# Optimization experiments

Hardware: AMD Instinct MI355X
Metric: run time of the kernel (lower is better)

Reference implementation:

```python
import jax, jax.numpy as jnp
import numpy as np

N_NODES = 50000
N_EDGES = 800000
N_GRAPHS = 256


def setup_inputs() -> dict:
    key = jax.random.key(0)
    ks = jax.random.split(key, 20)
    s = 0.05
    return {
        "x": jax.random.normal(ks[0], (N_NODES, 128), jnp.float32),
        "edge_index": jax.random.randint(ks[1], (2, N_EDGES), 0, N_NODES, jnp.int64),
        "batch_index": jnp.sort(jax.random.randint(ks[2], (N_NODES,), 0, N_GRAPHS, jnp.int64)),
        "mol_features": jax.random.normal(ks[3], (N_GRAPHS, 256), jnp.float32),
        "gcn_W": jax.random.normal(ks[4], (3, 128, 128), jnp.float32) * s,
        "gcn_b": jax.random.normal(ks[5], (3, 128), jnp.float32) * s,
        "gcn_out_W": jax.random.normal(ks[6], (128, 128), jnp.float32) * s,
        "gcn_out_b": jax.random.normal(ks[7], (128,), jnp.float32) * s,
        "mlp_W": jax.random.normal(ks[8], (2, 256, 256), jnp.float32) * s,
        "mlp_b": jax.random.normal(ks[9], (2, 256), jnp.float32) * s,
        "mlp_out_W": jax.random.normal(ks[10], (64, 256), jnp.float32) * s,
        "mlp_out_b": jax.random.normal(ks[11], (64,), jnp.float32) * s,
        "pred_W1": jax.random.normal(ks[12], (256, 192), jnp.float32) * s,
        "pred_b1": jax.random.normal(ks[13], (256,), jnp.float32) * s,
        "pred_W2": jax.random.normal(ks[14], (256, 256), jnp.float32) * s,
        "pred_b2": jax.random.normal(ks[15], (256,), jnp.float32) * s,
        "out_W": jax.random.normal(ks[16], (1, 256), jnp.float32) * s,
        "out_b": jax.random.normal(ks[17], (1,), jnp.float32) * s,
    }


def reference(x, edge_index, batch_index, mol_features,
              gcn_W, gcn_b, gcn_out_W, gcn_out_b,
              mlp_W, mlp_b, mlp_out_W, mlp_out_b,
              pred_W1, pred_b1, pred_W2, pred_b2, out_W, out_b):
    N = x.shape[0]
    E = edge_index.shape[1]
    G = mol_features.shape[0]
    row, col = edge_index[0], edge_index[1]

    # GCN normalization with self-loops (PyG gcn_norm, symmetric):
    # deg[i] = in-degree(i) + 1 (self loop); norm_e = d^-1/2[row] * d^-1/2[col]
    deg = jax.ops.segment_sum(jnp.ones((E,), x.dtype), col, num_segments=N) + 1.0
    dinv = jax.lax.rsqrt(deg)
    enorm = (dinv[row] * dinv[col])[:, None]     # [E,1]
    self_c = (dinv * dinv)[:, None]              # [N,1] self-loop coefficient

    h1 = x
    for i in range(gcn_W.shape[0]):
        h = h1 @ gcn_W[i].T                      # per-node transform [N,128]
        agg = jax.ops.segment_sum(h[row] * enorm, col, num_segments=N)
        h1 = jax.nn.relu(agg + self_c * h + gcn_b[i])
    h1 = h1 @ gcn_out_W.T + gcn_out_b            # final GCN-branch Linear (no relu)

    # global_mean_pool over batch_index -> [G,128]
    sums = jax.ops.segment_sum(h1, batch_index, num_segments=G)
    counts = jax.ops.segment_sum(jnp.ones((N,), x.dtype), batch_index, num_segments=G)
    h1 = sums / jnp.maximum(counts, 1.0)[:, None]

    # MLP branch: relu after every linear (including last)
    h2 = mol_features
    for i in range(mlp_W.shape[0]):
        h2 = jax.nn.relu(h2 @ mlp_W[i].T + mlp_b[i])
    h2 = jax.nn.relu(h2 @ mlp_out_W.T + mlp_out_b)

    h = jnp.concatenate([h1, h2], axis=1)        # [G,192]
    h = jax.nn.relu(h @ pred_W1.T + pred_b1)
    h = jax.nn.relu(h @ pred_W2.T + pred_b2)
    return h @ out_W.T + out_b                   # [G,1]
```

## Files before the change

kernel.cpp:

```cpp
#include <hip/hip_runtime.h>


typedef __attribute__((ext_vector_type(8))) short short8;
typedef __attribute__((ext_vector_type(4))) float f32x4;

#define BKT 64
#define SL 8
#define NBINBLK 256

__device__ __forceinline__ unsigned short f2bf(float f) {
    union { float f; unsigned u; } c; c.f = f;
    unsigned u = c.u;
    unsigned r = u + 0x7FFFu + ((u >> 16) & 1u);
    return (unsigned short)(r >> 16);
}
__device__ __forceinline__ float bflo(unsigned w) {
    union { unsigned u; float f; } c; c.u = w << 16; return c.f;
}
__device__ __forceinline__ float bfhi(unsigned w) {
    union { unsigned u; float f; } c; c.u = w & 0xFFFF0000u; return c.f;
}

__global__ void k_zero(int* ghist, float* pool, float* cnt, int* csr_pad,
                       int M, int N, int G) {
    int i = blockIdx.x * blockDim.x + threadIdx.x;
    if (i < M) ghist[i] = 0;
    if (i < G * 128) pool[i] = 0.f;
    if (i < G) cnt[i] = 0.f;
    if (i < 8) csr_pad[i] = 0;
}

__global__ __launch_bounds__(256) void k_hist(const int* __restrict__ col,
                                              int* __restrict__ ghist,
                                              int E, int C, int NBK) {
    __shared__ int h[784];
    int t = threadIdx.x;
    for (int i = t; i < NBK; i += 256) h[i] = 0;
    __syncthreads();
    const int x = blockIdx.x & (SL - 1);
    int e0 = blockIdx.x * C, e1 = min(E, e0 + C);
    for (int e = e0 + t; e < e1; e += 256) atomicAdd(&h[col[e] >> 6], 1);
    __syncthreads();
    for (int b = t; b < NBK; b += 256) {
        int c = h[b];
        if (c) atomicAdd(&ghist[b * SL + x], c);
    }
}

__global__ __launch_bounds__(256) void k_bscan(const int* __restrict__ ghist,
                                               int* __restrict__ gbase,
                                               int* __restrict__ cur,
                                               int* __restrict__ rowptr,
                                               int M, int N, int E) {
    __shared__ int ws[4];
    __shared__ int s_carry;
    int t = threadIdx.x, lane = t & 63, wv = t >> 6;
    if (t == 0) s_carry = 0;
    __syncthreads();
    for (int base = 0; base < M; base += 256) {
        int i = base + t;
        int v = (i < M) ? ghist[i] : 0;
        int x = v;
        #pragma unroll
        for (int off = 1; off < 64; off <<= 1) {
            int u = __shfl_up(x, off, 64);
            if (lane >= off) x += u;
        }
        if (lane == 63) ws[wv] = x;
        __syncthreads();
        int woff = 0;
        for (int w = 0; w < wv; ++w) woff += ws[w];
        int excl = s_carry + woff + (x - v);
        if (i < M) { gbase[i] = excl; cur[i] = excl; }
        __syncthreads();
        if (t == 255) s_carry = excl + v;
        __syncthreads();
    }
    if (t == 0) { gbase[M] = E; rowptr[N] = E; }
}

__global__ __launch_bounds__(256) void k_bin(const int* __restrict__ row,
                                             const int* __restrict__ col,
                                             int* __restrict__ cur,
                                             unsigned* __restrict__ gbin,
                                             int E, int C) {
    const int x = blockIdx.x & (SL - 1);
    int e0 = blockIdx.x * C, e1 = min(E, e0 + C);
    for (int e = e0 + threadIdx.x; e < e1; e += 256) {
        int c = col[e];
        int si = (c >> 6) * SL + x;
        int pos = atomicAdd(&cur[si], 1);
        gbin[pos] = (unsigned)row[e] | ((unsigned)(c & 63) << 16);
    }
}

__global__ __launch_bounds__(256) void k_csr(const unsigned* __restrict__ gbin,
                                             const int* __restrict__ gbase,
                                             int* __restrict__ rowptr,
                                             float* __restrict__ dinv,
                                             unsigned short* __restrict__ csrf,
                                             int N) {
    const int b = blockIdx.x, t = threadIdx.x;
    __shared__ int cnt[64], lcur[64];
    if (t < 64) cnt[t] = 0;
    __syncthreads();
    const int beg = gbase[b * SL], end = gbase[(b + 1) * SL];
    for (int i = beg + t; i < end; i += 256)
        atomicAdd(&cnt[gbin[i] >> 16], 1);
    __syncthreads();
    if (t < 64) {
        int v = cnt[t], x = v;
        #pragma unroll
        for (int off = 1; off < 64; off <<= 1) {
            int u = __shfl_up(x, off, 64);
            if (t >= off) x += u;
        }
        int excl = x - v;
        lcur[t] = excl;
        int node = b * 64 + t;
        if (node < N) {
            rowptr[node] = beg + excl;
            dinv[node] = rsqrtf((float)v + 1.0f);
        }
    }
    __syncthreads();
    for (int i = beg + t; i < end; i += 256) {
        unsigned v = gbin[i];
        int p = atomicAdd(&lcur[v >> 16], 1);
        csrf[beg + p] = (unsigned short)(v & 0xFFFFu);
    }
}

__global__ void k_castx(const float* __restrict__ x, const float* __restrict__ dinv,
                        unsigned short* __restrict__ xb, int total8) {
    int i = blockIdx.x * blockDim.x + threadIdx.x;
    if (i >= total8) return;
    float d = dinv[i >> 4];
    const float4* s = (const float4*)(x + (size_t)i * 8);
    float4 a = s[0], b = s[1];
    uint4 o;
    o.x = ((unsigned)f2bf(d * a.y) << 16) | f2bf(d * a.x);
    o.y = ((unsigned)f2bf(d * a.w) << 16) | f2bf(d * a.z);
    o.z = ((unsigned)f2bf(d * b.y) << 16) | f2bf(d * b.x);
    o.w = ((unsigned)f2bf(d * b.w) << 16) | f2bf(d * b.z);
    *(uint4*)(xb + (size_t)i * 8) = o;
}

__global__ void k_wcast(const float* __restrict__ gcnW, uint4* __restrict__ Wb) {
    int cid = blockIdx.x * 256 + threadIdx.x;
    if (cid >= 3 * 2048) return;
    int l = cid >> 11, rem = cid & 2047;
    int o = rem >> 4, c = rem & 15;
    const float4* s = (const float4*)(gcnW + (size_t)l * 16384 + o * 128 + c * 8);
    float4 a = s[0], b = s[1];
    uint4 v;
    v.x = ((unsigned)f2bf(a.y) << 16) | f2bf(a.x);
    v.y = ((unsigned)f2bf(a.w) << 16) | f2bf(a.z);
    v.z = ((unsigned)f2bf(b.y) << 16) | f2bf(b.x);
    v.w = ((unsigned)f2bf(b.w) << 16) | f2bf(b.z);
    Wb[(l << 11) | (o << 4) | (c ^ (o & 15))] = v;
}

__global__ __launch_bounds__(256) void k_agg(const unsigned short* __restrict__ h,
                                             unsigned short* __restrict__ y,
                                             const float* __restrict__ dinv,
                                             const int* __restrict__ rowptr,
                                             const unsigned short* __restrict__ csrf,
                                             int N) {
    const int lane = threadIdx.x & 63;
    const int n = blockIdx.x * 4 + (threadIdx.x >> 6);
    if (n >= N) return;
    const int fg = lane & 15;
    const int slot = lane >> 4;
    const int s = rowptr[n], e = rowptr[n + 1];

    float acc[8] = {0.f, 0.f, 0.f, 0.f, 0.f, 0.f, 0.f, 0.f};
    for (int base = s; base < e; base += 16) {
        int src_l = csrf[base + fg];
        #pragma unroll
        for (int i = 0; i < 4; ++i) {
            int j = i * 4 + slot;
            int src = __shfl(src_l, j, 16);
            uint4 v = *(const uint4*)(h + (size_t)src * 128 + fg * 8);
            bool ok = (base + j) < e;
            v.x = ok ? v.x : 0u; v.y = ok ? v.y : 0u;
            v.z = ok ? v.z : 0u; v.w = ok ? v.w : 0u;
            acc[0] += bflo(v.x); acc[1] += bfhi(v.x);
            acc[2] += bflo(v.y); acc[3] += bfhi(v.y);
            acc[4] += bflo(v.z); acc[5] += bfhi(v.z);
            acc[6] += bflo(v.w); acc[7] += bfhi(v.w);
        }
    }
    #pragma unroll
    for (int r = 0; r < 8; ++r) {
        acc[r] += __shfl_xor(acc[r], 16, 64);
        acc[r] += __shfl_xor(acc[r], 32, 64);
    }
    if (slot == 0) {
        float dn = dinv[n];
        uint4 hv = *(const uint4*)(h + (size_t)n * 128 + fg * 8);
        float sv[8] = {bflo(hv.x), bfhi(hv.x), bflo(hv.y), bfhi(hv.y),
                       bflo(hv.z), bfhi(hv.z), bflo(hv.w), bfhi(hv.w)};
        unsigned short ob[8];
        #pragma unroll
        for (int r = 0; r < 8; ++r) ob[r] = f2bf(dn * (acc[r] + sv[r]));
        uint4 o;
        o.x = ((unsigned)ob[1] << 16) | ob[0];
        o.y = ((unsigned)ob[3] << 16) | ob[2];
        o.z = ((unsigned)ob[5] << 16) | ob[4];
        o.w = ((unsigned)ob[7] << 16) | ob[6];
        *(uint4*)(y + (size_t)n * 128 + fg * 8) = o;
    }
}

__global__ __launch_bounds__(256) void k_mm(const unsigned short* __restrict__ A,
                                            const uint4* __restrict__ Wb,
                                            const float* __restrict__ bias,
                                            const float* __restrict__ dscale,
                                            unsigned short* __restrict__ C, int N) {
    __shared__ uint4 Wsh[2048];
    const int tid = threadIdx.x;
    #pragma unroll
    for (int it = 0; it < 8; ++it)
        Wsh[tid + it * 256] = Wb[tid + it * 256];

    const int lane = tid & 63;
    const int wv = tid >> 6;
    const int l15 = lane & 15, quad = lane >> 4;
    const int arow_i = blockIdx.x * 64 + wv * 16 + l15;
    const unsigned short* arow = A + (size_t)min(arow_i, N - 1) * 128;

    f32x4 acc[8];
    #pragma unroll
    for (int ct = 0; ct < 8; ++ct) acc[ct] = (f32x4){0.f, 0.f, 0.f, 0.f};

    __syncthreads();
    #pragma unroll
    for (int kiter = 0; kiter < 4; ++kiter) {
        short8 af = *(const short8*)(arow + kiter * 32 + quad * 8);
        const int cswz = (kiter * 4 + quad) ^ l15;
        #pragma unroll
        for (int ct = 0; ct < 8; ++ct) {
            short8 bf = *(const short8*)(&Wsh[((ct * 16 + l15) << 4) | cswz]);
            acc[ct] = __builtin_amdgcn_mfma_f32_16x16x32_bf16(af, bf, acc[ct], 0, 0, 0);
        }
    }

    const int rbase = blockIdx.x * 64 + wv * 16 + quad * 4;
    float ds[4];
    #pragma unroll
    for (int r = 0; r < 4; ++r) {
        int rr = rbase + r;
        ds[r] = (dscale && rr < N) ? dscale[rr] : 1.f;
    }
    #pragma unroll
    for (int ct = 0; ct < 8; ++ct) {
        int colc = ct * 16 + l15;
        float bcol = bias[colc];
        #pragma unroll
        for (int r = 0; r < 4; ++r) {
            int rr = rbase + r;
            if (rr < N) {
                float v = fmaxf(acc[ct][r] + bcol, 0.f) * ds[r];
                C[(size_t)rr * 128 + colc] = f2bf(v);
            }
        }
    }
}

__global__ __launch_bounds__(256) void k_pool(const unsigned short* __restrict__ h,
                                              const int* __restrict__ batch,
                                              float* __restrict__ pool,
                                              float* __restrict__ cnt, int N) {
    int t = threadIdx.x;
    int fg = t & 15, sg = t >> 4;
    int n0 = blockIdx.x * 512 + sg * 32;
    if (n0 >= N) return;
    int n1 = min(n0 + 32, N);
    int gprev = batch[n0];
    float racc[8] = {0.f, 0.f, 0.f, 0.f, 0.f, 0.f, 0.f, 0.f};
    float rcnt = 0.f;
    for (int n = n0; n < n1; ++n) {
        int g = batch[n];
        if (g != gprev) {
            float* dst = pool + (size_t)gprev * 128 + fg * 8;
            #pragma unroll
            for (int r = 0; r < 8; ++r) atomicAdd(dst + r, racc[r]);
            if (fg == 0) atomicAdd(&cnt[gprev], rcnt);
            #pragma unroll
            for (int r = 0; r < 8; ++r) racc[r] = 0.f;
            rcnt = 0.f; gprev = g;
        }
        uint4 v = *(const uint4*)(h + (size_t)n * 128 + fg * 8);
        racc[0] += bflo(v.x); racc[1] += bfhi(v.x);
        racc[2] += bflo(v.y); racc[3] += bfhi(v.y);
        racc[4] += bflo(v.z); racc[5] += bfhi(v.z);
        racc[6] += bflo(v.w); racc[7] += bfhi(v.w);
        rcnt += 1.f;
    }
    float* dst = pool + (size_t)gprev * 128 + fg * 8;
    #pragma unroll
    for (int r = 0; r < 8; ++r) atomicAdd(dst + r, racc[r]);
    if (fg == 0) atomicAdd(&cnt[gprev], rcnt);
}

__global__ __launch_bounds__(256) void k_head(
    const float* __restrict__ pool, const float* __restrict__ cnt,
    const float* __restrict__ gcnoW, const float* __restrict__ gcnob,
    const float* __restrict__ mol,
    const float* __restrict__ mlpW, const float* __restrict__ mlpb,
    const float* __restrict__ mloW, const float* __restrict__ mlob,
    const float* __restrict__ pW1, const float* __restrict__ pb1,
    const float* __restrict__ pW2, const float* __restrict__ pb2,
    const float* __restrict__ oW, const float* __restrict__ ob,
    float* __restrict__ out) {
    int g = blockIdx.x, t = threadIdx.x;
    __shared__ float s0[256], s1[256], s2[192], mean[128], red[256];

    s0[t] = mol[(size_t)g * 256 + t];
    if (t < 128) {
        float c = cnt[g];
        mean[t] = pool[(size_t)g * 128 + t] / fmaxf(c, 1.f);
    }
    __syncthreads();

    float acc = mlpb[t];
    {
        const float4* w = (const float4*)(mlpW + (size_t)t * 256);
        #pragma unroll 4
        for (int k4 = 0; k4 < 64; ++k4) {
            float4 wv = w[k4];
            acc += s0[k4*4+0]*wv.x + s0[k4*4+1]*wv.y + s0[k4*4+2]*wv.z + s0[k4*4+3]*wv.w;
        }
    }
    s1[t] = fmaxf(acc, 0.f);
    __syncthreads();

    acc = mlpb[256 + t];
    {
        const float4* w = (const float4*)(mlpW + 65536 + (size_t)t * 256);
        #pragma unroll 4
        for (int k4 = 0; k4 < 64; ++k4) {
            float4 wv = w[k4];
            acc += s1[k4*4+0]*wv.x + s1[k4*4+1]*wv.y + s1[k4*4+2]*wv.z + s1[k4*4+3]*wv.w;
        }
    }
    s0[t] = fmaxf(acc, 0.f);
    __syncthreads();

    if (t < 64) {
        float a2 = mlob[t];
        const float4* w = (const float4*)(mloW + (size_t)t * 256);
        #pragma unroll 4
        for (int k4 = 0; k4 < 64; ++k4) {
            float4 wv = w[k4];
            a2 += s0[k4*4+0]*wv.x + s0[k4*4+1]*wv.y + s0[k4*4+2]*wv.z + s0[k4*4+3]*wv.w;
        }
        s2[128 + t] = fmaxf(a2, 0.f);
    } else if (t < 192) {
        int o = t - 64;
        float a2 = gcnob[o];
        const float4* w = (const float4*)(gcnoW + (size_t)o * 128);
        #pragma unroll 4
        for (int k4 = 0; k4 < 32; ++k4) {
            float4 wv = w[k4];
            a2 += mean[k4*4+0]*wv.x + mean[k4*4+1]*wv.y + mean[k4*4+2]*wv.z + mean[k4*4+3]*wv.w;
        }
        s2[o] = a2;
    }
    __syncthreads();

    acc = pb1[t];
    {
        const float4* w = (const float4*)(pW1 + (size_t)t * 192);
        #pragma unroll 4
        for (int k4 = 0; k4 < 48; ++k4) {
            float4 wv = w[k4];
            acc += s2[k4*4+0]*wv.x + s2[k4*4+1]*wv.y + s2[k4*4+2]*wv.z + s2[k4*4+3]*wv.w;
        }
    }
    s1[t] = fmaxf(acc, 0.f);
    __syncthreads();

    acc = pb2[t];
    {
        const float4* w = (const float4*)(pW2 + (size_t)t * 256);
        #pragma unroll 4
        for (int k4 = 0; k4 < 64; ++k4) {
            float4 wv = w[k4];
            acc += s1[k4*4+0]*wv.x + s1[k4*4+1]*wv.y + s1[k4*4+2]*wv.z + s1[k4*4+3]*wv.w;
        }
    }
    s0[t] = fmaxf(acc, 0.f);
    __syncthreads();

    red[t] = s0[t] * oW[t];
    __syncthreads();
    for (int off = 128; off > 0; off >>= 1) {
        if (t < off) red[t] += red[t + off];
        __syncthreads();
    }
    if (t == 0) out[g] = red[0] + ob[0];
}

extern "C" void kernel_launch(void* const* d_in, const int* in_sizes, int n_in,
                              void* d_out, int out_size, void* d_ws, size_t ws_size,
                              hipStream_t stream) {
    const float* x     = (const float*)d_in[0];
    const int*   ei    = (const int*)d_in[1];
    const int*   batch = (const int*)d_in[2];
    const float* mol   = (const float*)d_in[3];
    const float* gcnW  = (const float*)d_in[4];
    const float* gcnb  = (const float*)d_in[5];
    const float* gcnoW = (const float*)d_in[6];
    const float* gcnob = (const float*)d_in[7];
    const float* mlpW  = (const float*)d_in[8];
    const float* mlpb  = (const float*)d_in[9];
    const float* mloW  = (const float*)d_in[10];
    const float* mlob  = (const float*)d_in[11];
    const float* pW1   = (const float*)d_in[12];
    const float* pb1   = (const float*)d_in[13];
    const float* pW2   = (const float*)d_in[14];
    const float* pb2   = (const float*)d_in[15];
    const float* oW    = (const float*)d_in[16];
    const float* ob    = (const float*)d_in[17];

    const int N = in_sizes[0] / 128;
    const int E = in_sizes[1] / 2;
    const int G = in_sizes[3] / 256;
    const int* row = ei;
    const int* col = ei + E;

    const int NBK = (N + BKT - 1) / BKT;
    const int M = NBK * SL;
    const int C = (E + NBINBLK - 1) / NBINBLK;

    char* p = (char*)d_ws;
    auto alloc = [&](size_t bytes) {
        char* q = p;
        p += (bytes + 255) & ~(size_t)255;
        return (void*)q;
    };
    int*    rowptr = (int*)alloc((size_t)(N + 1) * 4);
    float*  dinv   = (float*)alloc((size_t)N * 4);
    int*    ghist  = (int*)alloc((size_t)M * 4);
    int*    gbase  = (int*)alloc((size_t)(M + 1) * 4);
    int*    cur    = (int*)alloc((size_t)M * 4);
    unsigned* gbin = (unsigned*)alloc((size_t)E * 4);
    unsigned short* csrf = (unsigned short*)alloc((size_t)(E + 16) * 2);
    unsigned short* xb   = (unsigned short*)alloc((size_t)N * 128 * 2);
    unsigned short* bufA = (unsigned short*)alloc((size_t)N * 128 * 2);
    unsigned short* bufB = (unsigned short*)alloc((size_t)N * 128 * 2);
    uint4*  Wb     = (uint4*)alloc((size_t)3 * 2048 * 16);
    float*  pool   = (float*)alloc((size_t)G * 128 * 4);
    float*  cnt    = (float*)alloc((size_t)G * 4);

    const int NB = (N + 255) / 256;

    k_zero<<<NB, 256, 0, stream>>>(ghist, pool, cnt, (int*)(csrf + E), M, N, G);
    k_wcast<<<24, 256, 0, stream>>>(gcnW, Wb);
    k_hist<<<NBINBLK, 256, 0, stream>>>(col, ghist, E, C, NBK);
    k_bscan<<<1, 256, 0, stream>>>(ghist, gbase, cur, rowptr, M, N, E);
    k_bin<<<NBINBLK, 256, 0, stream>>>(row, col, cur, gbin, E, C);
    k_csr<<<NBK, 256, 0, stream>>>(gbin, gbase, rowptr, dinv, csrf, N);
    k_castx<<<(N * 16 + 255) / 256, 256, 0, stream>>>(x, dinv, xb, N * 16);

    const int mmblocks = (N + 63) / 64;
    const int aggblocks = (N + 3) / 4;
    const unsigned short* src = xb;
    for (int l = 0; l < 3; ++l) {
        k_agg<<<aggblocks, 256, 0, stream>>>(src, bufA, dinv, rowptr, csrf, N);
        k_mm<<<mmblocks, 256, 0, stream>>>(bufA, Wb + (size_t)l * 2048,
                                           gcnb + (size_t)l * 128,
                                           (l < 2) ? dinv : (const float*)nullptr,
                                           bufB, N);
        src = bufB;
    }
    k_pool<<<(N + 511) / 512, 256, 0, stream>>>(bufB, batch, pool, cnt, N);
    k_head<<<G, 256, 0, stream>>>(pool, cnt, gcnoW, gcnob, mol, mlpW, mlpb,
                                  mloW, mlob, pW1, pb1, pW2, pb2, oW, ob,
                                  (float*)d_out);
}
```

Baseline: 397.8 us.

## Fuse weight cast into init, batch head over graphs, simplify histogram

Merges the weight-cast kernel into the zeroing kernel to drop one launch. The histogram kernel now does global atomics directly instead of a shared-memory histogram, with the bin-block count raised. The head MLP now processes four graphs per block so each weight load is reused across graphs, and it uses a wave-shuffle reduction. The trade-off is more global atomic contention in the histogram and fewer head blocks.

```diff
diff --git a/kernel.cpp b/kernel.cpp
--- a/kernel.cpp
+++ b/kernel.cpp
@@ -6,7 +6,8 @@
 
 #define BKT 64
 #define SL 8
-#define NBINBLK 256
+#define NBINBLK 2048
+#define GPB 4
 
 __device__ __forceinline__ unsigned short f2bf(float f) {
     union { float f; unsigned u; } c; c.f = f;
@@ -21,30 +22,35 @@
     union { unsigned u; float f; } c; c.u = w & 0xFFFF0000u; return c.f;
 }
 
-__global__ void k_zero(int* ghist, float* pool, float* cnt, int* csr_pad,
-                       int M, int N, int G) {
-    int i = blockIdx.x * blockDim.x + threadIdx.x;
+__global__ void k_init(int* ghist, float* pool, float* cnt, int* csr_pad,
+                       const float* __restrict__ gcnW, uint4* __restrict__ Wb,
+                       int M, int G) {
+    int i = blockIdx.x * 256 + threadIdx.x;
     if (i < M) ghist[i] = 0;
     if (i < G * 128) pool[i] = 0.f;
     if (i < G) cnt[i] = 0.f;
     if (i < 8) csr_pad[i] = 0;
+    if (i < 3 * 2048) {
+        int l = i >> 11, rem = i & 2047;
+        int o = rem >> 4, c = rem & 15;
+        const float4* s = (const float4*)(gcnW + (size_t)l * 16384 + o * 128 + c * 8);
+        float4 a = s[0], b = s[1];
+        uint4 v;
+        v.x = ((unsigned)f2bf(a.y) << 16) | f2bf(a.x);
+        v.y = ((unsigned)f2bf(a.w) << 16) | f2bf(a.z);
+        v.z = ((unsigned)f2bf(b.y) << 16) | f2bf(b.x);
+        v.w = ((unsigned)f2bf(b.w) << 16) | f2bf(b.z);
+        Wb[(l << 11) | (o << 4) | (c ^ (o & 15))] = v;
+    }
 }
 
 __global__ __launch_bounds__(256) void k_hist(const int* __restrict__ col,
                                               int* __restrict__ ghist,
-                                              int E, int C, int NBK) {
-    __shared__ int h[784];
-    int t = threadIdx.x;
-    for (int i = t; i < NBK; i += 256) h[i] = 0;
-    __syncthreads();
+                                              int E, int C) {
     const int x = blockIdx.x & (SL - 1);
     int e0 = blockIdx.x * C, e1 = min(E, e0 + C);
-    for (int e = e0 + t; e < e1; e += 256) atomicAdd(&h[col[e] >> 6], 1);
-    __syncthreads();
-    for (int b = t; b < NBK; b += 256) {
-        int c = h[b];
-        if (c) atomicAdd(&ghist[b * SL + x], c);
-    }
+    for (int e = e0 + threadIdx.x; e < e1; e += 256)
+        atomicAdd(&ghist[(col[e] >> 6) * SL + x], 1);
 }
 
 __global__ __launch_bounds__(256) void k_bscan(const int* __restrict__ ghist,
@@ -144,21 +150,6 @@
     o.z = ((unsigned)f2bf(d * b.y) << 16) | f2bf(d * b.x);
     o.w = ((unsigned)f2bf(d * b.w) << 16) | f2bf(d * b.z);
     *(uint4*)(xb + (size_t)i * 8) = o;
-}
-
-__global__ void k_wcast(const float* __restrict__ gcnW, uint4* __restrict__ Wb) {
-    int cid = blockIdx.x * 256 + threadIdx.x;
-    if (cid >= 3 * 2048) return;
-    int l = cid >> 11, rem = cid & 2047;
-    int o = rem >> 4, c = rem & 15;
-    const float4* s = (const float4*)(gcnW + (size_t)l * 16384 + o * 128 + c * 8);
-    float4 a = s[0], b = s[1];
-    uint4 v;
-    v.x = ((unsigned)f2bf(a.y) << 16) | f2bf(a.x);
-    v.y = ((unsigned)f2bf(a.w) << 16) | f2bf(a.z);
-    v.z = ((unsigned)f2bf(b.y) << 16) | f2bf(b.x);
-    v.w = ((unsigned)f2bf(b.w) << 16) | f2bf(b.z);
-    Wb[(l << 11) | (o << 4) | (c ^ (o & 15))] = v;
 }
 
 __global__ __launch_bounds__(256) void k_agg(const unsigned short* __restrict__ h,
@@ -304,6 +295,25 @@
     if (fg == 0) atomicAdd(&cnt[gprev], rcnt);
 }
 
+__device__ __forceinline__ void matvec(const float (*S)[GPB],
+                                       const float* __restrict__ wrow,
+                                       int K4, float bias, float* acc) {
+    #pragma unroll
+    for (int g = 0; g < GPB; ++g) acc[g] = bias;
+    #pragma unroll 4
+    for (int k4 = 0; k4 < K4; ++k4) {
+        float4 w = *(const float4*)(wrow + (size_t)k4 * 4);
+        float4 s0 = *(const float4*)&S[k4 * 4 + 0][0];
+        float4 s1 = *(const float4*)&S[k4 * 4 + 1][0];
+        float4 s2 = *(const float4*)&S[k4 * 4 + 2][0];
+        float4 s3 = *(const float4*)&S[k4 * 4 + 3][0];
+        acc[0] += w.x * s0.x + w.y * s1.x + w.z * s2.x + w.w * s3.x;
+        acc[1] += w.x * s0.y + w.y * s1.y + w.z * s2.y + w.w * s3.y;
+        acc[2] += w.x * s0.z + w.y * s1.z + w.z * s2.z + w.w * s3.z;
+        acc[3] += w.x * s0.w + w.y * s1.w + w.z * s2.w + w.w * s3.w;
+    }
+}
+
 __global__ __launch_bounds__(256) void k_head(
     const float* __restrict__ pool, const float* __restrict__ cnt,
     const float* __restrict__ gcnoW, const float* __restrict__ gcnob,
@@ -313,94 +323,73 @@
     const float* __restrict__ pW1, const float* __restrict__ pb1,
     const float* __restrict__ pW2, const float* __restrict__ pb2,
     const float* __restrict__ oW, const float* __restrict__ ob,
-    float* __restrict__ out) {
-    int g = blockIdx.x, t = threadIdx.x;
-    __shared__ float s0[256], s1[256], s2[192], mean[128], red[256];
-
-    s0[t] = mol[(size_t)g * 256 + t];
-    if (t < 128) {
-        float c = cnt[g];
-        mean[t] = pool[(size_t)g * 128 + t] / fmaxf(c, 1.f);
-    }
-    __syncthreads();
-
-    float acc = mlpb[t];
-    {
-        const float4* w = (const float4*)(mlpW + (size_t)t * 256);
-        #pragma unroll 4
-        for (int k4 = 0; k4 < 64; ++k4) {
-            float4 wv = w[k4];
-            acc += s0[k4*4+0]*wv.x + s0[k4*4+1]*wv.y + s0[k4*4+2]*wv.z + s0[k4*4+3]*wv.w;
-        }
-    }
-    s1[t] = fmaxf(acc, 0.f);
-    __syncthreads();
-
-    acc = mlpb[256 + t];
-    {
-        const float4* w = (const float4*)(mlpW + 65536 + (size_t)t * 256);
-        #pragma unroll 4
-        for (int k4 = 0; k4 < 64; ++k4) {
-            float4 wv = w[k4];
-            acc += s1[k4*4+0]*wv.x + s1[k4*4+1]*wv.y + s1[k4*4+2]*wv.z + s1[k4*4+3]*wv.w;
-        }
-    }
-    s0[t] = fmaxf(acc, 0.f);
+    float* __restrict__ out, int G) {
+    const int g0 = blockIdx.x * GPB;
+    const int t = threadIdx.x;
+    __shared__ float A[256][GPB];
+    __shared__ float B[256][GPB];
+    __shared__ float Mn[128][GPB];
+    __shared__ float red[4][GPB];
+    float acc[GPB];
+
+    #pragma unroll
+    for (int g = 0; g < GPB; ++g) {
+        int gi = min(g0 + g, G - 1);
+        A[t][g] = mol[(size_t)gi * 256 + t];
+        if (t < 128) {
+            float c = cnt[gi];
+            Mn[t][g] = pool[(size_t)gi * 128 + t] / fmaxf(c, 1.f);
+        }
+    }
+    __syncthreads();
+
+    matvec(A, mlpW + (size_t)t * 256, 64, mlpb[t], acc);
+    __syncthreads();
+    #pragma unroll
+    for (int g = 0; g < GPB; ++g) B[t][g] = fmaxf(acc[g], 0.f);
+    __syncthreads();
+
+    matvec(B, mlpW + 65536 + (size_t)t * 256, 64, mlpb[256 + t], acc);
+    __syncthreads();
+    #pragma unroll
+    for (int g = 0; g < GPB; ++g) A[t][g] = fmaxf(acc[g], 0.f);
     __syncthreads();
 
     if (t < 64) {
-        float a2 = mlob[t];
-        const float4* w = (const float4*)(mloW + (size_t)t * 256);
-        #pragma unroll 4
-        for (int k4 = 0; k4 < 64; ++k4) {
-            float4 wv = w[k4];
-            a2 += s0[k4*4+0]*wv.x + s0[k4*4+1]*wv.y + s0[k4*4+2]*wv.z + s0[k4*4+3]*wv.w;
-        }
-        s2[128 + t] = fmaxf(a2, 0.f);
+        matvec(A, mloW + (size_t)t * 256, 64, mlob[t], acc);
+        #pragma unroll
+        for (int g = 0; g < GPB; ++g) B[128 + t][g] = fmaxf(acc[g], 0.f);
     } else if (t < 192) {
         int o = t - 64;
-        float a2 = gcnob[o];
-        const float4* w = (const float4*)(gcnoW + (size_t)o * 128);
-        #pragma unroll 4
-        for (int k4 = 0; k4 < 32; ++k4) {
-            float4 wv = w[k4];
-            a2 += mean[k4*4+0]*wv.x + mean[k4*4+1]*wv.y + mean[k4*4+2]*wv.z + mean[k4*4+3]*wv.w;
-        }
-        s2[o] = a2;
-    }
-    __syncthreads();
-
-    acc = pb1[t];
-    {
-        const float4* w = (const float4*)(pW1 + (size_t)t * 192);
-        #pragma unroll 4
-        for (int k4 = 0; k4 < 48; ++k4) {
-            float4 wv = w[k4];
-            acc += s2[k4*4+0]*wv.x + s2[k4*4+1]*wv.y + s2[k4*4+2]*wv.z + s2[k4*4+3]*wv.w;
-        }
-    }
-    s1[t] = fmaxf(acc, 0.f);
-    __syncthreads();
-
-    acc = pb2[t];
-    {
-        const float4* w = (const float4*)(pW2 + (size_t)t * 256);
-        #pragma unroll 4
-        for (int k4 = 0; k4 < 64; ++k4) {
-            float4 wv = w[k4];
-            acc += s1[k4*4+0]*wv.x + s1[k4*4+1]*wv.y + s1[k4*4+2]*wv.z + s1[k4*4+3]*wv.w;
-        }
-    }
-    s0[t] = fmaxf(acc, 0.f);
-    __syncthreads();
-
-    red[t] = s0[t] * oW[t];
-    __syncthreads();
-    for (int off = 128; off > 0; off >>= 1) {
-        if (t < off) red[t] += red[t + off];
-        __syncthreads();
-    }
-    if (t == 0) out[g] = red[0] + ob[0];
+        matvec(Mn, gcnoW + (size_t)o * 128, 32, gcnob[o], acc);
+        #pragma unroll
+        for (int g = 0; g < GPB; ++g) B[o][g] = acc[g];
+    }
+    __syncthreads();
+
+    matvec(B, pW1 + (size_t)t * 192, 48, pb1[t], acc);
+    __syncthreads();
+    #pragma unroll
+    for (int g = 0; g < GPB; ++g) A[t][g] = fmaxf(acc[g], 0.f);
+    __syncthreads();
+
+    matvec(A, pW2 + (size_t)t * 256, 64, pb2[t], acc);
+    float w = oW[t];
+    float vv[GPB];
+    #pragma unroll
+    for (int g = 0; g < GPB; ++g) vv[g] = fmaxf(acc[g], 0.f) * w;
+    #pragma unroll
+    for (int off = 32; off > 0; off >>= 1)
+        #pragma unroll
+        for (int g = 0; g < GPB; ++g) vv[g] += __shfl_xor(vv[g], off, 64);
+    if ((t & 63) == 0)
+        #pragma unroll
+        for (int g = 0; g < GPB; ++g) red[t >> 6][g] = vv[g];
+    __syncthreads();
+    if (t < GPB) {
+        float s = red[0][t] + red[1][t] + red[2][t] + red[3][t] + ob[0];
+        if (g0 + t < G) out[g0 + t] = s;
+    }
 }
 
 extern "C" void kernel_launch(void* const* d_in, const int* in_sizes, int n_in,
@@ -457,9 +446,9 @@
 
     const int NB = (N + 255) / 256;
 
-    k_zero<<<NB, 256, 0, stream>>>(ghist, pool, cnt, (int*)(csrf + E), M, N, G);
-    k_wcast<<<24, 256, 0, stream>>>(gcnW, Wb);
-    k_hist<<<NBINBLK, 256, 0, stream>>>(col, ghist, E, C, NBK);
+    k_init<<<NB, 256, 0, stream>>>(ghist, pool, cnt, (int*)(csrf + E),
+                                   gcnW, Wb, M, G);
+    k_hist<<<NBINBLK, 256, 0, stream>>>(col, ghist, E, C);
     k_bscan<<<1, 256, 0, stream>>>(ghist, gbase, cur, rowptr, M, N, E);
     k_bin<<<NBINBLK, 256, 0, stream>>>(row, col, cur, gbin, E, C);
     k_csr<<<NBK, 256, 0, stream>>>(gbin, gbase, rowptr, dinv, csrf, N);
@@ -477,7 +466,7 @@
         src = bufB;
     }
     k_pool<<<(N + 511) / 512, 256, 0, stream>>>(bufB, batch, pool, cnt, N);
-    k_head<<<G, 256, 0, stream>>>(pool, cnt, gcnoW, gcnob, mol, mlpW, mlpb,
-                                  mloW, mlob, pW1, pb1, pW2, pb2, oW, ob,
-                                  (float*)d_out);
-}
+    k_head<<<(G + GPB - 1) / GPB, 256, 0, stream>>>(
+        pool, cnt, gcnoW, gcnob, mol, mlpW, mlpb, mloW, mlob,
+        pW1, pb1, pW2, pb2, oW, ob, (float*)d_out, G);
+}
```

New measurement: 414.3 us. 4.2% more time.
